# Kernel optimization log

Measured on AMD Instinct MI355X. Metric: run time of the kernel, lower is better.

The kernel has to match this reference:

```python
import jax, jax.numpy as jnp
import numpy as np

IN_NF, IN_EF, OUT_NF, H1, H2, H_IN = 16, 8, 16, 8, 8, 16
N_NODES, N_EDGES = 100000, 2000000


def _mlp(x, w1, b1, w2, b2):
    # Linear -> LeakyReLU(0.2) -> Linear
    return jax.nn.leaky_relu(x @ w1 + b1, negative_slope=0.2) @ w2 + b2


def setup_inputs() -> dict:
    key = jax.random.key(0)
    ks = jax.random.split(key, 20)
    d_in = 2 * IN_NF + IN_EF  # 40
    inp = {
        "nf": jax.random.normal(ks[0], (N_NODES, IN_NF), jnp.float32),
        "src_out": jax.random.randint(ks[1], (N_EDGES,), 0, N_NODES),
        "dst_out": jax.random.randint(ks[2], (N_EDGES,), 0, N_NODES),
        "nef_out": jax.random.normal(ks[3], (N_EDGES, IN_EF), jnp.float32),
        "src_in": jax.random.randint(ks[4], (N_EDGES,), 0, N_NODES),
        "dst_in": jax.random.randint(ks[5], (N_EDGES,), 0, N_NODES),
        "nef_in": jax.random.normal(ks[6], (N_EDGES, IN_EF), jnp.float32),
        # MLP_msg_o2i: (2*in_nf+in_ef) -> h_in -> out_nf
        "w_o2i1": jax.random.normal(ks[7], (d_in, H_IN), jnp.float32) * 0.1,
        "b_o2i1": jnp.zeros((H_IN,), jnp.float32),
        "w_o2i2": jax.random.normal(ks[8], (H_IN, OUT_NF), jnp.float32) * 0.1,
        "b_o2i2": jnp.zeros((OUT_NF,), jnp.float32),
        # MLP_msg_i2o: (2*in_nf+in_ef) -> h_in -> 1+h1+h2
        "w_i2o1": jax.random.normal(ks[9], (d_in, H_IN), jnp.float32) * 0.1,
        "b_i2o1": jnp.zeros((H_IN,), jnp.float32),
        "w_i2o2": jax.random.normal(ks[10], (H_IN, 1 + H1 + H2), jnp.float32) * 0.1,
        "b_i2o2": jnp.zeros((1 + H1 + H2,), jnp.float32),
        # MLP_reduce_o: (in_nf+h1+h2) -> h_in -> out_nf  (note: in_nf==out_nf here)
        "w_red1": jax.random.normal(ks[11], (OUT_NF + H1 + H2, H_IN), jnp.float32) * 0.1,
        "b_red1": jnp.zeros((H_IN,), jnp.float32),
        "w_red2": jax.random.normal(ks[12], (H_IN, OUT_NF), jnp.float32) * 0.1,
        "b_red2": jnp.zeros((OUT_NF,), jnp.float32),
    }
    return inp


def reference(nf, src_out, dst_out, nef_out, src_in, dst_in, nef_in,
              w_o2i1, b_o2i1, w_o2i2, b_o2i2,
              w_i2o1, b_i2o1, w_i2o2, b_i2o2,
              w_red1, b_red1, w_red2, b_red2):
    n = nf.shape[0]
    # --- update_all over 'net_out': edge gather-concat -> MLP -> scatter sum
    x_o = jnp.concatenate([nf[src_out], nf[dst_out], nef_out], axis=1)  # [E, 40]
    efi = _mlp(x_o, w_o2i1, b_o2i1, w_o2i2, b_o2i2)                      # [E, out_nf]
    new_nf = jax.ops.segment_sum(efi, dst_out, num_segments=n)           # overwrites 'new_nf'
    # --- apply_edges over 'net_in': gated messages
    x_i = jnp.concatenate([nf[src_in], nf[dst_in], nef_in], axis=1)      # [E, 40]
    m = _mlp(x_i, w_i2o1, b_i2o1, w_i2o2, b_i2o2)                        # [E, 1+h1+h2]
    k = jax.nn.sigmoid(m[:, :1])
    efo1 = m[:, 1:1 + H1] * k
    efo2 = m[:, 1 + H1:] * k
    # --- scatter sum / mean into dst nodes
    nfo1 = jax.ops.segment_sum(efo1, dst_in, num_segments=n)
    cnt = jax.ops.segment_sum(jnp.ones((dst_in.shape[0],), nf.dtype), dst_in, num_segments=n)
    nfo2 = jax.ops.segment_sum(efo2, dst_in, num_segments=n) / jnp.maximum(cnt, 1.0)[:, None]
    # --- apply_nodes only on net_in destination nodes; others keep new_nf
    reduced = _mlp(jnp.concatenate([new_nf, nfo1, nfo2], axis=1), w_red1, b_red1, w_red2, b_red2)
    has_in = (cnt > 0)[:, None]
    return jnp.where(has_in, reduced, new_nf)
```

## Files before the change

kernel.cpp:

```cpp
#include <hip/hip_runtime.h>
#include <math.h>

#define IN_NF 16
#define IN_EF 8
#define OUT_NF 16
#define H1 8
#define H2 8
#define H_IN 16
#define D_IN 40
#define NT 4
#define SCAN_NB 128

typedef unsigned int uivec4 __attribute__((ext_vector_type(4)));

__device__ __forceinline__ unsigned int f2bf_bits(float f) {
    unsigned int u = __float_as_uint(f);
    u += 0x7FFFu + ((u >> 16) & 1u);
    return u >> 16;
}
__device__ __forceinline__ float bf_lo(unsigned int w) { return __uint_as_float(w << 16); }
__device__ __forceinline__ float bf_hi(unsigned int w) { return __uint_as_float(w & 0xFFFF0000u); }

__global__ __launch_bounds__(256) void k_pre(
    const float* __restrict__ nf, unsigned short* __restrict__ nf16, int n_nodes,
    const int* __restrict__ dst_out, const int* __restrict__ dst_in,
    int* __restrict__ curA, int* __restrict__ curB, int n_edges, int nb_conv)
{
    if ((int)blockIdx.x < nb_conv) {
        int n = blockIdx.x * 256 + threadIdx.x;
        if (n >= n_nodes) return;
        const float4* p = (const float4*)(nf + (long)n * IN_NF);
        unsigned int w[8];
#pragma unroll
        for (int q = 0; q < 4; ++q) {
            float4 v = p[q];
            w[2*q+0] = f2bf_bits(v.x) | (f2bf_bits(v.y) << 16);
            w[2*q+1] = f2bf_bits(v.z) | (f2bf_bits(v.w) << 16);
        }
        uint4* o = (uint4*)(nf16 + (size_t)n * 16);
        o[0] = make_uint4(w[0], w[1], w[2], w[3]);
        o[1] = make_uint4(w[4], w[5], w[6], w[7]);
    } else {
        int i = ((blockIdx.x - nb_conv) * 256 + threadIdx.x) * 4;
        if (i + 3 < n_edges) {
            int4 a = *(const int4*)(dst_out + i);
            atomicAdd(&curA[a.x], 1); atomicAdd(&curA[a.y], 1);
            atomicAdd(&curA[a.z], 1); atomicAdd(&curA[a.w], 1);
            int4 b = *(const int4*)(dst_in + i);
            atomicAdd(&curB[b.x], 1); atomicAdd(&curB[b.y], 1);
            atomicAdd(&curB[b.z], 1); atomicAdd(&curB[b.w], 1);
        } else {
            for (int e = i; e < n_edges; ++e) {
                atomicAdd(&curA[dst_out[e]], 1);
                atomicAdd(&curB[dst_in[e]], 1);
            }
        }
    }
}

__global__ __launch_bounds__(256) void k_hist(
    const int* __restrict__ dst_out, const int* __restrict__ dst_in,
    int* __restrict__ off_out, int* __restrict__ off_in, int n_edges)
{
    int i = (blockIdx.x * blockDim.x + threadIdx.x) * 4;
    if (i + 3 < n_edges) {
        int4 a = *(const int4*)(dst_out + i);
        atomicAdd(&off_out[a.x], 1); atomicAdd(&off_out[a.y], 1);
        atomicAdd(&off_out[a.z], 1); atomicAdd(&off_out[a.w], 1);
        int4 b = *(const int4*)(dst_in + i);
        atomicAdd(&off_in[b.x], 1); atomicAdd(&off_in[b.y], 1);
        atomicAdd(&off_in[b.z], 1); atomicAdd(&off_in[b.w], 1);
    } else {
        for (int e = i; e < n_edges; ++e) {
            atomicAdd(&off_out[dst_out[e]], 1);
            atomicAdd(&off_in[dst_in[e]], 1);
        }
    }
}

__global__ __launch_bounds__(256) void k_scan_partial(
    const int* __restrict__ a0, const int* __restrict__ a1, int n,
    int* __restrict__ bsum)
{
    int arr = blockIdx.x >> 7;
    int blk = blockIdx.x & (SCAN_NB - 1);
    const int* a = arr ? a1 : a0;
    int chunk = (n + SCAN_NB - 1) / SCAN_NB;
    int beg = blk * chunk;
    int end = min(beg + chunk, n);
    int s = 0;
    for (int i = beg + threadIdx.x; i < end; i += 256) s += a[i];
    __shared__ int sm[256];
    int t = threadIdx.x;
    sm[t] = s;
    __syncthreads();
    for (int d = 128; d > 0; d >>= 1) {
        if (t < d) sm[t] += sm[t + d];
        __syncthreads();
    }
    if (t == 0) bsum[arr * SCAN_NB + blk] = sm[0];
}

__global__ __launch_bounds__(64) void k_scan_bsum(int* __restrict__ bsum)
{
    int arr = threadIdx.x;
    if (arr >= 2) return;
    int run = 0;
    for (int i = 0; i < SCAN_NB; ++i) {
        int v = bsum[arr * SCAN_NB + i];
        bsum[arr * SCAN_NB + i] = run;
        run += v;
    }
}

__global__ __launch_bounds__(256) void k_scan_final(
    int* __restrict__ a0, int* __restrict__ a1, int n,
    const int* __restrict__ bsum)
{
    int arr = blockIdx.x >> 7;
    int blk = blockIdx.x & (SCAN_NB - 1);
    int* a = arr ? a1 : a0;
    int chunk = (n + SCAN_NB - 1) / SCAN_NB;
    int beg = blk * chunk;
    int end = min(beg + chunk, n);
    int t = threadIdx.x;
    __shared__ int sm[256];
    __shared__ int carry_sm;
    if (t == 0) carry_sm = bsum[arr * SCAN_NB + blk];
    __syncthreads();
    for (int base = beg; base < end; base += 256) {
        int i = base + t;
        int v = (i < end) ? a[i] : 0;
        sm[t] = v;
        __syncthreads();
        for (int d = 1; d < 256; d <<= 1) {
            int u = (t >= d) ? sm[t - d] : 0;
            __syncthreads();
            sm[t] += u;
            __syncthreads();
        }
        int carry = carry_sm;
        if (i < end) a[i] = carry + sm[t] - v;
        __syncthreads();
        if (t == 0) carry_sm = carry + sm[255];
        __syncthreads();
    }
}

__global__ __launch_bounds__(256, 4) void k_edges(
    const unsigned short* __restrict__ nf16,
    const int* __restrict__ srcA, const int* __restrict__ dstA,
    const float* __restrict__ nefA,
    const int* __restrict__ srcB, const int* __restrict__ dstB,
    const float* __restrict__ nefB,
    const float* __restrict__ W1A, const float* __restrict__ B1A,
    const float* __restrict__ W2A, const float* __restrict__ B2A,
    const float* __restrict__ W1B, const float* __restrict__ B1B,
    const float* __restrict__ W2B, const float* __restrict__ B2B,
    int* __restrict__ curA, int* __restrict__ curB,
    unsigned short* __restrict__ msgA, unsigned short* __restrict__ msgB,
    int n_edges, int nbe)
{
    bool isA = (int)blockIdx.x < nbe;
    int bid = isA ? (int)blockIdx.x : (int)blockIdx.x - nbe;
    int e = bid * 256 + (int)threadIdx.x;
    if (e >= n_edges) return;

    const int* src = isA ? srcA : srcB;
    const int* dst = isA ? dstA : dstB;
    const float* nef = isA ? nefA : nefB;
    const float* W1 = isA ? W1A : W1B;
    const float* B1 = isA ? B1A : B1B;
    int* cursor = isA ? curA : curB;
    unsigned short* msg = isA ? msgA : msgB;

    int s = src[e];
    int d = dst[e];

    const uint4* pS = (const uint4*)(nf16 + (size_t)s * 16);
    uint4 Sa = pS[0], Sb = pS[1];
    const uint4* pD = (const uint4*)(nf16 + (size_t)d * 16);
    uint4 Da = pD[0], Db = pD[1];
    const float4* pN = (const float4*)(nef + (size_t)e * IN_EF);
    float4 Na = pN[0], Nb = pN[1];

    int slot = atomicAdd(&cursor[d], 1);

    float h[H_IN];
#pragma unroll
    for (int j = 0; j < H_IN; ++j) h[j] = B1[j];
    {
        unsigned int wS[8] = {Sa.x,Sa.y,Sa.z,Sa.w,Sb.x,Sb.y,Sb.z,Sb.w};
        unsigned int wD[8] = {Da.x,Da.y,Da.z,Da.w,Db.x,Db.y,Db.z,Db.w};
#pragma unroll
        for (int w = 0; w < 8; ++w) {
            float a0 = bf_lo(wS[w]), a1 = bf_hi(wS[w]);
            float b0 = bf_lo(wD[w]), b1 = bf_hi(wD[w]);
            const float* r0 = W1 + (2*w) * H_IN;
            const float* r1 = W1 + (2*w+1) * H_IN;
            const float* r2 = W1 + (IN_NF + 2*w) * H_IN;
            const float* r3 = W1 + (IN_NF + 2*w+1) * H_IN;
#pragma unroll
            for (int j = 0; j < H_IN; ++j) {
                h[j] = fmaf(a0, r0[j], h[j]);
                h[j] = fmaf(a1, r1[j], h[j]);
                h[j] = fmaf(b0, r2[j], h[j]);
                h[j] = fmaf(b1, r3[j], h[j]);
            }
        }
        float nv[8] = {Na.x,Na.y,Na.z,Na.w,Nb.x,Nb.y,Nb.z,Nb.w};
#pragma unroll
        for (int k = 0; k < IN_EF; ++k) {
            const float* r = W1 + (2*IN_NF + k) * H_IN;
            float a0 = nv[k];
#pragma unroll
            for (int j = 0; j < H_IN; ++j) h[j] = fmaf(a0, r[j], h[j]);
        }
    }
#pragma unroll
    for (int j = 0; j < H_IN; ++j) h[j] = (h[j] >= 0.f) ? h[j] : 0.2f * h[j];

    unsigned int w[8];
    if (isA) {
        float o[OUT_NF];
#pragma unroll
        for (int j = 0; j < OUT_NF; ++j) o[j] = B2A[j];
#pragma unroll
        for (int k = 0; k < H_IN; ++k) {
            float hk = h[k];
            const float* r = W2A + k * OUT_NF;
#pragma unroll
            for (int j = 0; j < OUT_NF; ++j) o[j] = fmaf(hk, r[j], o[j]);
        }
#pragma unroll
        for (int q = 0; q < 8; ++q)
            w[q] = f2bf_bits(o[2*q]) | (f2bf_bits(o[2*q+1]) << 16);
    } else {
        const int M = 1 + H1 + H2;
        float o[17];
#pragma unroll
        for (int j = 0; j < M; ++j) o[j] = B2B[j];
#pragma unroll
        for (int k = 0; k < H_IN; ++k) {
            float hk = h[k];
            const float* r = W2B + k * M;
#pragma unroll
            for (int j = 0; j < M; ++j) o[j] = fmaf(hk, r[j], o[j]);
        }
        float g = 1.f / (1.f + __expf(-o[0]));
#pragma unroll
        for (int q = 0; q < 8; ++q)
            w[q] = f2bf_bits(o[1+2*q] * g) | (f2bf_bits(o[2+2*q] * g) << 16);
    }

    uivec4* pm = (uivec4*)(msg + (size_t)slot * 16);
    uivec4 v0 = {w[0], w[1], w[2], w[3]};
    uivec4 v1 = {w[4], w[5], w[6], w[7]};
    __builtin_nontemporal_store(v0, pm);
    __builtin_nontemporal_store(v1, pm + 1);
}

__global__ __launch_bounds__(256, 4) void k_gather(
    const int* __restrict__ curA, const int* __restrict__ curB,
    const unsigned short* __restrict__ msgA, const unsigned short* __restrict__ msgB,
    const float* __restrict__ w_red1, const float* __restrict__ b_red1,
    const float* __restrict__ w_red2, const float* __restrict__ b_red2,
    float* __restrict__ out, int n_nodes)
{
    int tid = blockIdx.x * blockDim.x + threadIdx.x;
    int node = tid >> 2;
    int t = tid & (NT - 1);
    if (node >= n_nodes) return;

    int begA = (node == 0) ? 0 : curA[node - 1];
    int endA = curA[node];
    int begB = (node == 0) ? 0 : curB[node - 1];
    int endB = curB[node];

    float accA[16], accB[16];
#pragma unroll
    for (int j = 0; j < 16; ++j) { accA[j] = 0.f; accB[j] = 0.f; }

    for (int i = begA + t; i < endA; i += NT) {
        const uint4* p = (const uint4*)(msgA + (size_t)i * 16);
        uint4 v0 = p[0], v1 = p[1];
        unsigned int w0=v0.x,w1=v0.y,w2=v0.z,w3=v0.w,w4=v1.x,w5=v1.y,w6=v1.z,w7=v1.w;
        accA[0]+=bf_lo(w0); accA[1]+=bf_hi(w0); accA[2]+=bf_lo(w1); accA[3]+=bf_hi(w1);
        accA[4]+=bf_lo(w2); accA[5]+=bf_hi(w2); accA[6]+=bf_lo(w3); accA[7]+=bf_hi(w3);
        accA[8]+=bf_lo(w4); accA[9]+=bf_hi(w4); accA[10]+=bf_lo(w5); accA[11]+=bf_hi(w5);
        accA[12]+=bf_lo(w6); accA[13]+=bf_hi(w6); accA[14]+=bf_lo(w7); accA[15]+=bf_hi(w7);
    }
    for (int i = begB + t; i < endB; i += NT) {
        const uint4* p = (const uint4*)(msgB + (size_t)i * 16);
        uint4 v0 = p[0], v1 = p[1];
        unsigned int w0=v0.x,w1=v0.y,w2=v0.z,w3=v0.w,w4=v1.x,w5=v1.y,w6=v1.z,w7=v1.w;
        accB[0]+=bf_lo(w0); accB[1]+=bf_hi(w0); accB[2]+=bf_lo(w1); accB[3]+=bf_hi(w1);
        accB[4]+=bf_lo(w2); accB[5]+=bf_hi(w2); accB[6]+=bf_lo(w3); accB[7]+=bf_hi(w3);
        accB[8]+=bf_lo(w4); accB[9]+=bf_hi(w4); accB[10]+=bf_lo(w5); accB[11]+=bf_hi(w5);
        accB[12]+=bf_lo(w6); accB[13]+=bf_hi(w6); accB[14]+=bf_lo(w7); accB[15]+=bf_hi(w7);
    }

#pragma unroll
    for (int mask = 1; mask < NT; mask <<= 1) {
#pragma unroll
        for (int j = 0; j < 16; ++j) {
            accA[j] += __shfl_xor(accA[j], mask);
            accB[j] += __shfl_xor(accB[j], mask);
        }
    }
    if (t != 0) return;

    int deg = endB - begB;
    float inv = 1.f / fmaxf((float)deg, 1.f);
    float x2[32];
#pragma unroll
    for (int j = 0; j < 16; ++j) x2[j] = accA[j];
#pragma unroll
    for (int j = 0; j < H1; ++j) x2[16 + j] = accB[j];
#pragma unroll
    for (int j = 0; j < H2; ++j) x2[16 + H1 + j] = accB[8 + j] * inv;

    float h[H_IN];
#pragma unroll
    for (int j = 0; j < H_IN; ++j) h[j] = b_red1[j];
#pragma unroll
    for (int k = 0; k < 32; ++k) {
        float xk = x2[k];
#pragma unroll
        for (int j = 0; j < H_IN; ++j) h[j] = fmaf(xk, w_red1[k * H_IN + j], h[j]);
    }
#pragma unroll
    for (int j = 0; j < H_IN; ++j) h[j] = (h[j] >= 0.f) ? h[j] : 0.2f * h[j];

    float o[OUT_NF];
#pragma unroll
    for (int j = 0; j < OUT_NF; ++j) o[j] = b_red2[j];
#pragma unroll
    for (int k = 0; k < H_IN; ++k) {
        float hk = h[k];
#pragma unroll
        for (int j = 0; j < OUT_NF; ++j) o[j] = fmaf(hk, w_red2[k * OUT_NF + j], o[j]);
    }

    bool has_in = (deg > 0);
    float4* po = (float4*)(out + (long)node * OUT_NF);
#pragma unroll
    for (int i = 0; i < 4; ++i) {
        float4 v;
        if (has_in) { v.x=o[4*i+0]; v.y=o[4*i+1]; v.z=o[4*i+2]; v.w=o[4*i+3]; }
        else        { v.x=accA[4*i+0]; v.y=accA[4*i+1]; v.z=accA[4*i+2]; v.w=accA[4*i+3]; }
        po[i] = v;
    }
}

__global__ __launch_bounds__(256) void k_scatter(
    const int* __restrict__ dst_out, const int* __restrict__ dst_in,
    int* __restrict__ off_out, int* __restrict__ off_in,
    int* __restrict__ perm_out, int* __restrict__ perm_in, int n_edges)
{
    int e = blockIdx.x * blockDim.x + threadIdx.x;
    if (e >= n_edges) return;
    int p0 = atomicAdd(&off_out[dst_out[e]], 1);
    perm_out[p0] = e;
    int p1 = atomicAdd(&off_in[dst_in[e]], 1);
    perm_in[p1] = e;
}

__global__ __launch_bounds__(256) void k_node_fused(
    const float* __restrict__ nf,
    const int* __restrict__ src_out, const float* __restrict__ nef_out,
    const int* __restrict__ src_in, const float* __restrict__ nef_in,
    const int* __restrict__ off_out, const int* __restrict__ off_in,
    const int* __restrict__ perm_out, const int* __restrict__ perm_in,
    const float* __restrict__ w_o2i1, const float* __restrict__ b_o2i1,
    const float* __restrict__ w_o2i2, const float* __restrict__ b_o2i2,
    const float* __restrict__ w_i2o1, const float* __restrict__ b_i2o1,
    const float* __restrict__ w_i2o2, const float* __restrict__ b_i2o2,
    const float* __restrict__ w_red1, const float* __restrict__ b_red1,
    const float* __restrict__ w_red2, const float* __restrict__ b_red2,
    float* __restrict__ out, int n_nodes)
{
    int tid = blockIdx.x * blockDim.x + threadIdx.x;
    int node = tid >> 2;
    int t = tid & (NT - 1);
    if (node >= n_nodes) return;

    float xd[IN_NF];
    {
        const float4* p = (const float4*)(nf + (long)node * IN_NF);
#pragma unroll
        for (int i = 0; i < 4; ++i) {
            float4 v = p[i];
            xd[4*i+0]=v.x; xd[4*i+1]=v.y; xd[4*i+2]=v.z; xd[4*i+3]=v.w;
        }
    }
    float hbA[H_IN], hbB[H_IN];
#pragma unroll
    for (int j = 0; j < H_IN; ++j) { hbA[j] = b_o2i1[j]; hbB[j] = b_i2o1[j]; }
#pragma unroll
    for (int k = 0; k < IN_NF; ++k) {
        float xk = xd[k];
#pragma unroll
        for (int j = 0; j < H_IN; ++j) {
            hbA[j] = fmaf(xk, w_o2i1[(IN_NF + k) * H_IN + j], hbA[j]);
            hbB[j] = fmaf(xk, w_i2o1[(IN_NF + k) * H_IN + j], hbB[j]);
        }
    }

    float accA[OUT_NF];
#pragma unroll
    for (int j = 0; j < OUT_NF; ++j) accA[j] = 0.f;
    int begO = (node == 0) ? 0 : off_out[node - 1];
    int endO = off_out[node];
    int localO = 0;
    for (int i = begO + t; i < endO; i += NT) {
        int e = perm_out[i];
        int s = src_out[e];
        float xs[IN_NF], xe[IN_EF];
        {
            const float4* ps = (const float4*)(nf + (long)s * IN_NF);
#pragma unroll
            for (int q = 0; q < 4; ++q) {
                float4 v = ps[q];
                xs[4*q+0]=v.x; xs[4*q+1]=v.y; xs[4*q+2]=v.z; xs[4*q+3]=v.w;
            }
            const float4* pe = (const float4*)(nef_out + (long)e * IN_EF);
#pragma unroll
            for (int q = 0; q < 2; ++q) {
                float4 v = pe[q];
                xe[4*q+0]=v.x; xe[4*q+1]=v.y; xe[4*q+2]=v.z; xe[4*q+3]=v.w;
            }
        }
        float h[H_IN];
#pragma unroll
        for (int j = 0; j < H_IN; ++j) h[j] = hbA[j];
#pragma unroll
        for (int k = 0; k < IN_NF; ++k) {
            float xk = xs[k];
#pragma unroll
            for (int j = 0; j < H_IN; ++j) h[j] = fmaf(xk, w_o2i1[k * H_IN + j], h[j]);
        }
#pragma unroll
        for (int k = 0; k < IN_EF; ++k) {
            float xk = xe[k];
#pragma unroll
            for (int j = 0; j < H_IN; ++j) h[j] = fmaf(xk, w_o2i1[(2*IN_NF + k) * H_IN + j], h[j]);
        }
#pragma unroll
        for (int j = 0; j < H_IN; ++j) h[j] = (h[j] >= 0.f) ? h[j] : 0.2f * h[j];
#pragma unroll
        for (int k = 0; k < H_IN; ++k) {
            float hk = h[k];
#pragma unroll
            for (int j = 0; j < OUT_NF; ++j) accA[j] = fmaf(hk, w_o2i2[k * OUT_NF + j], accA[j]);
        }
        ++localO;
    }
#pragma unroll
    for (int j = 0; j < OUT_NF; ++j) accA[j] = fmaf((float)localO, b_o2i2[j], accA[j]);

    float acc1[H1], acc2[H2];
#pragma unroll
    for (int j = 0; j < H1; ++j) acc1[j] = 0.f;
#pragma unroll
    for (int j = 0; j < H2; ++j) acc2[j] = 0.f;
    int begI = (node == 0) ? 0 : off_in[node - 1];
    int endI = off_in[node];
    int deg = endI - begI;
    for (int i = begI + t; i < endI; i += NT) {
        int e = perm_in[i];
        int s = src_in[e];
        float xs[IN_NF], xe[IN_EF];
        {
            const float4* ps = (const float4*)(nf + (long)s * IN_NF);
#pragma unroll
            for (int q = 0; q < 4; ++q) {
                float4 v = ps[q];
                xs[4*q+0]=v.x; xs[4*q+1]=v.y; xs[4*q+2]=v.z; xs[4*q+3]=v.w;
            }
            const float4* pe = (const float4*)(nef_in + (long)e * IN_EF);
#pragma unroll
            for (int q = 0; q < 2; ++q) {
                float4 v = pe[q];
                xe[4*q+0]=v.x; xe[4*q+1]=v.y; xe[4*q+2]=v.z; xe[4*q+3]=v.w;
            }
        }
        float h[H_IN];
#pragma unroll
        for (int j = 0; j < H_IN; ++j) h[j] = hbB[j];
#pragma unroll
        for (int k = 0; k < IN_NF; ++k) {
            float xk = xs[k];
#pragma unroll
            for (int j = 0; j < H_IN; ++j) h[j] = fmaf(xk, w_i2o1[k * H_IN + j], h[j]);
        }
#pragma unroll
        for (int k = 0; k < IN_EF; ++k) {
            float xk = xe[k];
#pragma unroll
            for (int j = 0; j < H_IN; ++j) h[j] = fmaf(xk, w_i2o1[(2*IN_NF + k) * H_IN + j], h[j]);
        }
#pragma unroll
        for (int j = 0; j < H_IN; ++j) h[j] = (h[j] >= 0.f) ? h[j] : 0.2f * h[j];

        const int M = 1 + H1 + H2;
        float o[17];
#pragma unroll
        for (int j = 0; j < M; ++j) o[j] = b_i2o2[j];
#pragma unroll
        for (int k = 0; k < H_IN; ++k) {
            float hk = h[k];
#pragma unroll
            for (int j = 0; j < M; ++j) o[j] = fmaf(hk, w_i2o2[k * M + j], o[j]);
        }
        float gate = 1.f / (1.f + __expf(-o[0]));
#pragma unroll
        for (int j = 0; j < H1; ++j) acc1[j] = fmaf(o[1 + j], gate, acc1[j]);
#pragma unroll
        for (int j = 0; j < H2; ++j) acc2[j] = fmaf(o[1 + H1 + j], gate, acc2[j]);
    }

#pragma unroll
    for (int mask = 1; mask < NT; mask <<= 1) {
#pragma unroll
        for (int j = 0; j < OUT_NF; ++j) accA[j] += __shfl_xor(accA[j], mask);
#pragma unroll
        for (int j = 0; j < H1; ++j) acc1[j] += __shfl_xor(acc1[j], mask);
#pragma unroll
        for (int j = 0; j < H2; ++j) acc2[j] += __shfl_xor(acc2[j], mask);
    }
    if (t != 0) return;

    float inv = 1.f / fmaxf((float)deg, 1.f);
    float x2[32];
#pragma unroll
    for (int j = 0; j < OUT_NF; ++j) x2[j] = accA[j];
#pragma unroll
    for (int j = 0; j < H1; ++j) x2[OUT_NF + j] = acc1[j];
#pragma unroll
    for (int j = 0; j < H2; ++j) x2[OUT_NF + H1 + j] = acc2[j] * inv;

    float h[H_IN];
#pragma unroll
    for (int j = 0; j < H_IN; ++j) h[j] = b_red1[j];
#pragma unroll
    for (int k = 0; k < 32; ++k) {
        float xk = x2[k];
#pragma unroll
        for (int j = 0; j < H_IN; ++j) h[j] = fmaf(xk, w_red1[k * H_IN + j], h[j]);
    }
#pragma unroll
    for (int j = 0; j < H_IN; ++j) h[j] = (h[j] >= 0.f) ? h[j] : 0.2f * h[j];

    float o[OUT_NF];
#pragma unroll
    for (int j = 0; j < OUT_NF; ++j) o[j] = b_red2[j];
#pragma unroll
    for (int k = 0; k < H_IN; ++k) {
        float hk = h[k];
#pragma unroll
        for (int j = 0; j < OUT_NF; ++j) o[j] = fmaf(hk, w_red2[k * OUT_NF + j], o[j]);
    }

    bool has_in = (deg > 0);
    float4* po = (float4*)(out + (long)node * OUT_NF);
#pragma unroll
    for (int i = 0; i < 4; ++i) {
        float4 v;
        if (has_in) { v.x=o[4*i+0]; v.y=o[4*i+1]; v.z=o[4*i+2]; v.w=o[4*i+3]; }
        else        { v.x=accA[4*i+0]; v.y=accA[4*i+1]; v.z=accA[4*i+2]; v.w=accA[4*i+3]; }
        po[i] = v;
    }
}

extern "C" void kernel_launch(void* const* d_in, const int* in_sizes, int n_in,
                              void* d_out, int out_size, void* d_ws, size_t ws_size,
                              hipStream_t stream) {
    const float* nf      = (const float*)d_in[0];
    const int*   src_out = (const int*)d_in[1];
    const int*   dst_out = (const int*)d_in[2];
    const float* nef_out = (const float*)d_in[3];
    const int*   src_in  = (const int*)d_in[4];
    const int*   dst_in  = (const int*)d_in[5];
    const float* nef_in  = (const float*)d_in[6];
    const float* w_o2i1  = (const float*)d_in[7];
    const float* b_o2i1  = (const float*)d_in[8];
    const float* w_o2i2  = (const float*)d_in[9];
    const float* b_o2i2  = (const float*)d_in[10];
    const float* w_i2o1  = (const float*)d_in[11];
    const float* b_i2o1  = (const float*)d_in[12];
    const float* w_i2o2  = (const float*)d_in[13];
    const float* b_i2o2  = (const float*)d_in[14];
    const float* w_red1  = (const float*)d_in[15];
    const float* b_red1  = (const float*)d_in[16];
    const float* w_red2  = (const float*)d_in[17];
    const float* b_red2  = (const float*)d_in[18];

    int n_nodes = in_sizes[0] / IN_NF;
    int n_edges = in_sizes[1];
    float* out = (float*)d_out;

    dim3 blk(256);
    dim3 egrid((n_edges + 255) / 256);
    dim3 hgrid((n_edges / 4 + 256) / 256 + 1);
    dim3 ngrid(((size_t)n_nodes * NT + 255) / 256);
    dim3 sgrid(2 * SCAN_NB);

    size_t off_bytes = (size_t)2 * n_nodes * sizeof(int);
    size_t nf16_bytes = (size_t)n_nodes * 16 * sizeof(unsigned short);
    size_t msg_bytes = (size_t)n_edges * 16 * sizeof(unsigned short);
    size_t need_fast = off_bytes + nf16_bytes + 2 * msg_bytes + 256;

    if (ws_size >= need_fast) {
        int* curA = (int*)d_ws;
        int* curB = curA + n_nodes;
        unsigned short* nf16 = (unsigned short*)(curB + n_nodes);
        unsigned short* msgA = nf16 + (size_t)n_nodes * 16;
        unsigned short* msgB = msgA + (size_t)n_edges * 16;
        int* bsum = (int*)msgA;

        int nb_conv = (n_nodes + 255) / 256;
        int nb_hist = (n_edges / 4 + 256) / 256 + 1;
        dim3 pgrid(nb_conv + nb_hist);

        int nbe = (n_edges + 255) / 256;
        dim3 edge_grid(2 * nbe);

        hipMemsetAsync(d_ws, 0, off_bytes, stream);
        k_pre<<<pgrid, blk, 0, stream>>>(nf, nf16, n_nodes, dst_out, dst_in,
                                         curA, curB, n_edges, nb_conv);
        k_scan_partial<<<sgrid, blk, 0, stream>>>(curA, curB, n_nodes, bsum);
        k_scan_bsum<<<dim3(1), dim3(64), 0, stream>>>(bsum);
        k_scan_final<<<sgrid, blk, 0, stream>>>(curA, curB, n_nodes, bsum);
        k_edges<<<edge_grid, blk, 0, stream>>>(nf16,
                                               src_out, dst_out, nef_out,
                                               src_in, dst_in, nef_in,
                                               w_o2i1, b_o2i1, w_o2i2, b_o2i2,
                                               w_i2o1, b_i2o1, w_i2o2, b_i2o2,
                                               curA, curB, msgA, msgB,
                                               n_edges, nbe);
        k_gather<<<ngrid, blk, 0, stream>>>(curA, curB, msgA, msgB,
                                            w_red1, b_red1, w_red2, b_red2,
                                            out, n_nodes);
    } else {
        int* off_out  = (int*)d_ws;
        int* off_in   = off_out + n_nodes;
        int* perm_out = off_in + n_nodes;
        int* perm_in  = perm_out + n_edges;
        int* bsum = perm_out;

        hipMemsetAsync(d_ws, 0, off_bytes, stream);
        k_hist<<<hgrid, blk, 0, stream>>>(dst_out, dst_in, off_out, off_in, n_edges);
        k_scan_partial<<<sgrid, blk, 0, stream>>>(off_out, off_in, n_nodes, bsum);
        k_scan_bsum<<<dim3(1), dim3(64), 0, stream>>>(bsum);
        k_scan_final<<<sgrid, blk, 0, stream>>>(off_out, off_in, n_nodes, bsum);
        k_scatter<<<egrid, blk, 0, stream>>>(dst_out, dst_in, off_out, off_in,
                                             perm_out, perm_in, n_edges);
        k_node_fused<<<ngrid, blk, 0, stream>>>(nf, src_out, nef_out, src_in, nef_in,
                                          off_out, off_in, perm_out, perm_in,
                                          w_o2i1, b_o2i1, w_o2i2, b_o2i2,
                                          w_i2o1, b_i2o1, w_i2o2, b_i2o2,
                                          w_red1, b_red1, w_red2, b_red2,
                                          out, n_nodes);
    }
}
```

Baseline: 458.5 us.

## Write edge messages in edge order and gather via inverse slot index

The edge kernel now writes each bf16 message at its own edge index in a plain streaming pattern, and it records the edge id at the node-sorted slot in a new inverse index array. The gather kernel then reads each node's messages through this index instead of reading a contiguous CSR-ordered buffer. The aim is to replace scattered 32-byte message stores with coalesced stores. In exchange the gather does indirect 32-byte reads, and each edge costs an extra 4-byte scattered write. The old CSR path is kept as the fallback when the workspace is too small, and the older perm-based fallback is removed.

```diff
diff --git a/kernel.cpp b/kernel.cpp
--- a/kernel.cpp
+++ b/kernel.cpp
@@ -7,7 +7,6 @@
 #define H1 8
 #define H2 8
 #define H_IN 16
-#define D_IN 40
 #define NT 4
 #define SCAN_NB 128
 
@@ -54,26 +53,6 @@
                 atomicAdd(&curA[dst_out[e]], 1);
                 atomicAdd(&curB[dst_in[e]], 1);
             }
-        }
-    }
-}
-
-__global__ __launch_bounds__(256) void k_hist(
-    const int* __restrict__ dst_out, const int* __restrict__ dst_in,
-    int* __restrict__ off_out, int* __restrict__ off_in, int n_edges)
-{
-    int i = (blockIdx.x * blockDim.x + threadIdx.x) * 4;
-    if (i + 3 < n_edges) {
-        int4 a = *(const int4*)(dst_out + i);
-        atomicAdd(&off_out[a.x], 1); atomicAdd(&off_out[a.y], 1);
-        atomicAdd(&off_out[a.z], 1); atomicAdd(&off_out[a.w], 1);
-        int4 b = *(const int4*)(dst_in + i);
-        atomicAdd(&off_in[b.x], 1); atomicAdd(&off_in[b.y], 1);
-        atomicAdd(&off_in[b.z], 1); atomicAdd(&off_in[b.w], 1);
-    } else {
-        for (int e = i; e < n_edges; ++e) {
-            atomicAdd(&off_out[dst_out[e]], 1);
-            atomicAdd(&off_in[dst_in[e]], 1);
         }
     }
 }
@@ -147,7 +126,231 @@
     }
 }
 
-__global__ __launch_bounds__(256, 4) void k_edges(
+__global__ __launch_bounds__(256, 4) void k_edges_stream(
+    const unsigned short* __restrict__ nf16,
+    const int* __restrict__ srcA, const int* __restrict__ dstA,
+    const float* __restrict__ nefA,
+    const int* __restrict__ srcB, const int* __restrict__ dstB,
+    const float* __restrict__ nefB,
+    const float* __restrict__ W1A, const float* __restrict__ B1A,
+    const float* __restrict__ W2A, const float* __restrict__ B2A,
+    const float* __restrict__ W1B, const float* __restrict__ B1B,
+    const float* __restrict__ W2B, const float* __restrict__ B2B,
+    int* __restrict__ curA, int* __restrict__ curB,
+    int* __restrict__ invA, int* __restrict__ invB,
+    unsigned short* __restrict__ msgA, unsigned short* __restrict__ msgB,
+    int n_edges, int nbe)
+{
+    bool isA = (int)blockIdx.x < nbe;
+    int bid = isA ? (int)blockIdx.x : (int)blockIdx.x - nbe;
+    int e = bid * 256 + (int)threadIdx.x;
+    if (e >= n_edges) return;
+
+    const int* src = isA ? srcA : srcB;
+    const int* dst = isA ? dstA : dstB;
+    const float* nef = isA ? nefA : nefB;
+    const float* W1 = isA ? W1A : W1B;
+    const float* B1 = isA ? B1A : B1B;
+    int* cursor = isA ? curA : curB;
+    int* inv = isA ? invA : invB;
+    unsigned short* msg = isA ? msgA : msgB;
+
+    int s = src[e];
+    int d = dst[e];
+
+    const uint4* pS = (const uint4*)(nf16 + (size_t)s * 16);
+    uint4 Sa = pS[0], Sb = pS[1];
+    const uint4* pD = (const uint4*)(nf16 + (size_t)d * 16);
+    uint4 Da = pD[0], Db = pD[1];
+    const float4* pN = (const float4*)(nef + (size_t)e * IN_EF);
+    float4 Na = pN[0], Nb = pN[1];
+
+    int slot = atomicAdd(&cursor[d], 1);
+
+    float h[H_IN];
+#pragma unroll
+    for (int j = 0; j < H_IN; ++j) h[j] = B1[j];
+    {
+        unsigned int wS[8] = {Sa.x,Sa.y,Sa.z,Sa.w,Sb.x,Sb.y,Sb.z,Sb.w};
+        unsigned int wD[8] = {Da.x,Da.y,Da.z,Da.w,Db.x,Db.y,Db.z,Db.w};
+#pragma unroll
+        for (int w = 0; w < 8; ++w) {
+            float a0 = bf_lo(wS[w]), a1 = bf_hi(wS[w]);
+            float b0 = bf_lo(wD[w]), b1 = bf_hi(wD[w]);
+            const float* r0 = W1 + (2*w) * H_IN;
+            const float* r1 = W1 + (2*w+1) * H_IN;
+            const float* r2 = W1 + (IN_NF + 2*w) * H_IN;
+            const float* r3 = W1 + (IN_NF + 2*w+1) * H_IN;
+#pragma unroll
+            for (int j = 0; j < H_IN; ++j) {
+                h[j] = fmaf(a0, r0[j], h[j]);
+                h[j] = fmaf(a1, r1[j], h[j]);
+                h[j] = fmaf(b0, r2[j], h[j]);
+                h[j] = fmaf(b1, r3[j], h[j]);
+            }
+        }
+        float nv[8] = {Na.x,Na.y,Na.z,Na.w,Nb.x,Nb.y,Nb.z,Nb.w};
+#pragma unroll
+        for (int k = 0; k < IN_EF; ++k) {
+            const float* r = W1 + (2*IN_NF + k) * H_IN;
+            float a0 = nv[k];
+#pragma unroll
+            for (int j = 0; j < H_IN; ++j) h[j] = fmaf(a0, r[j], h[j]);
+        }
+    }
+#pragma unroll
+    for (int j = 0; j < H_IN; ++j) h[j] = (h[j] >= 0.f) ? h[j] : 0.2f * h[j];
+
+    unsigned int w[8];
+    if (isA) {
+        float o[OUT_NF];
+#pragma unroll
+        for (int j = 0; j < OUT_NF; ++j) o[j] = B2A[j];
+#pragma unroll
+        for (int k = 0; k < H_IN; ++k) {
+            float hk = h[k];
+            const float* r = W2A + k * OUT_NF;
+#pragma unroll
+            for (int j = 0; j < OUT_NF; ++j) o[j] = fmaf(hk, r[j], o[j]);
+        }
+#pragma unroll
+        for (int q = 0; q < 8; ++q)
+            w[q] = f2bf_bits(o[2*q]) | (f2bf_bits(o[2*q+1]) << 16);
+    } else {
+        const int M = 1 + H1 + H2;
+        float o[17];
+#pragma unroll
+        for (int j = 0; j < M; ++j) o[j] = B2B[j];
+#pragma unroll
+        for (int k = 0; k < H_IN; ++k) {
+            float hk = h[k];
+            const float* r = W2B + k * M;
+#pragma unroll
+            for (int j = 0; j < M; ++j) o[j] = fmaf(hk, r[j], o[j]);
+        }
+        float g = 1.f / (1.f + __expf(-o[0]));
+#pragma unroll
+        for (int q = 0; q < 8; ++q)
+            w[q] = f2bf_bits(o[1+2*q] * g) | (f2bf_bits(o[2+2*q] * g) << 16);
+    }
+
+    uivec4* pm = (uivec4*)(msg + (size_t)e * 16);
+    uivec4 v0 = {w[0], w[1], w[2], w[3]};
+    uivec4 v1 = {w[4], w[5], w[6], w[7]};
+    __builtin_nontemporal_store(v0, pm);
+    __builtin_nontemporal_store(v1, pm + 1);
+    inv[slot] = e;
+}
+
+__global__ __launch_bounds__(256, 4) void k_gather_ind(
+    const int* __restrict__ curA, const int* __restrict__ curB,
+    const int* __restrict__ invA, const int* __restrict__ invB,
+    const unsigned short* __restrict__ msgA, const unsigned short* __restrict__ msgB,
+    const float* __restrict__ w_red1, const float* __restrict__ b_red1,
+    const float* __restrict__ w_red2, const float* __restrict__ b_red2,
+    float* __restrict__ out, int n_nodes)
+{
+    int tid = blockIdx.x * blockDim.x + threadIdx.x;
+    int node = tid >> 2;
+    int t = tid & (NT - 1);
+    if (node >= n_nodes) return;
+
+    int begA = (node == 0) ? 0 : curA[node - 1];
+    int endA = curA[node];
+    int begB = (node == 0) ? 0 : curB[node - 1];
+    int endB = curB[node];
+
+    float accA[16], accB[16];
+#pragma unroll
+    for (int j = 0; j < 16; ++j) { accA[j] = 0.f; accB[j] = 0.f; }
+
+    {
+        int i = begA + t;
+        int e = (i < endA) ? invA[i] : 0;
+        while (i < endA) {
+            int inext = i + NT;
+            int enext = (inext < endA) ? invA[inext] : 0;
+            const uint4* p = (const uint4*)(msgA + (size_t)e * 16);
+            uint4 v0 = p[0], v1 = p[1];
+            unsigned int w0=v0.x,w1=v0.y,w2=v0.z,w3=v0.w,w4=v1.x,w5=v1.y,w6=v1.z,w7=v1.w;
+            accA[0]+=bf_lo(w0); accA[1]+=bf_hi(w0); accA[2]+=bf_lo(w1); accA[3]+=bf_hi(w1);
+            accA[4]+=bf_lo(w2); accA[5]+=bf_hi(w2); accA[6]+=bf_lo(w3); accA[7]+=bf_hi(w3);
+            accA[8]+=bf_lo(w4); accA[9]+=bf_hi(w4); accA[10]+=bf_lo(w5); accA[11]+=bf_hi(w5);
+            accA[12]+=bf_lo(w6); accA[13]+=bf_hi(w6); accA[14]+=bf_lo(w7); accA[15]+=bf_hi(w7);
+            i = inext; e = enext;
+        }
+    }
+    {
+        int i = begB + t;
+        int e = (i < endB) ? invB[i] : 0;
+        while (i < endB) {
+            int inext = i + NT;
+            int enext = (inext < endB) ? invB[inext] : 0;
+            const uint4* p = (const uint4*)(msgB + (size_t)e * 16);
+            uint4 v0 = p[0], v1 = p[1];
+            unsigned int w0=v0.x,w1=v0.y,w2=v0.z,w3=v0.w,w4=v1.x,w5=v1.y,w6=v1.z,w7=v1.w;
+            accB[0]+=bf_lo(w0); accB[1]+=bf_hi(w0); accB[2]+=bf_lo(w1); accB[3]+=bf_hi(w1);
+            accB[4]+=bf_lo(w2); accB[5]+=bf_hi(w2); accB[6]+=bf_lo(w3); accB[7]+=bf_hi(w3);
+            accB[8]+=bf_lo(w4); accB[9]+=bf_hi(w4); accB[10]+=bf_lo(w5); accB[11]+=bf_hi(w5);
+            accB[12]+=bf_lo(w6); accB[13]+=bf_hi(w6); accB[14]+=bf_lo(w7); accB[15]+=bf_hi(w7);
+            i = inext; e = enext;
+        }
+    }
+
+#pragma unroll
+    for (int mask = 1; mask < NT; mask <<= 1) {
+#pragma unroll
+        for (int j = 0; j < 16; ++j) {
+            accA[j] += __shfl_xor(accA[j], mask);
+            accB[j] += __shfl_xor(accB[j], mask);
+        }
+    }
+    if (t != 0) return;
+
+    int deg = endB - begB;
+    float inv = 1.f / fmaxf((float)deg, 1.f);
+    float x2[32];
+#pragma unroll
+    for (int j = 0; j < 16; ++j) x2[j] = accA[j];
+#pragma unroll
+    for (int j = 0; j < H1; ++j) x2[16 + j] = accB[j];
+#pragma unroll
+    for (int j = 0; j < H2; ++j) x2[16 + H1 + j] = accB[8 + j] * inv;
+
+    float h[H_IN];
+#pragma unroll
+    for (int j = 0; j < H_IN; ++j) h[j] = b_red1[j];
+#pragma unroll
+    for (int k = 0; k < 32; ++k) {
+        float xk = x2[k];
+#pragma unroll
+        for (int j = 0; j < H_IN; ++j) h[j] = fmaf(xk, w_red1[k * H_IN + j], h[j]);
+    }
+#pragma unroll
+    for (int j = 0; j < H_IN; ++j) h[j] = (h[j] >= 0.f) ? h[j] : 0.2f * h[j];
+
+    float o[OUT_NF];
+#pragma unroll
+    for (int j = 0; j < OUT_NF; ++j) o[j] = b_red2[j];
+#pragma unroll
+    for (int k = 0; k < H_IN; ++k) {
+        float hk = h[k];
+#pragma unroll
+        for (int j = 0; j < OUT_NF; ++j) o[j] = fmaf(hk, w_red2[k * OUT_NF + j], o[j]);
+    }
+
+    bool has_in = (deg > 0);
+    float4* po = (float4*)(out + (long)node * OUT_NF);
+#pragma unroll
+    for (int i = 0; i < 4; ++i) {
+        float4 v;
+        if (has_in) { v.x=o[4*i+0]; v.y=o[4*i+1]; v.z=o[4*i+2]; v.w=o[4*i+3]; }
+        else        { v.x=accA[4*i+0]; v.y=accA[4*i+1]; v.z=accA[4*i+2]; v.w=accA[4*i+3]; }
+        po[i] = v;
+    }
+}
+
+__global__ __launch_bounds__(256, 4) void k_edges_csr(
     const unsigned short* __restrict__ nf16,
     const int* __restrict__ srcA, const int* __restrict__ dstA,
     const float* __restrict__ nefA,
@@ -260,7 +463,7 @@
     __builtin_nontemporal_store(v1, pm + 1);
 }
 
-__global__ __launch_bounds__(256, 4) void k_gather(
+__global__ __launch_bounds__(256, 4) void k_gather_csr(
     const int* __restrict__ curA, const int* __restrict__ curB,
     const unsigned short* __restrict__ msgA, const unsigned short* __restrict__ msgB,
     const float* __restrict__ w_red1, const float* __restrict__ b_red1,
@@ -319,226 +522,6 @@
     for (int j = 0; j < H1; ++j) x2[16 + j] = accB[j];
 #pragma unroll
     for (int j = 0; j < H2; ++j) x2[16 + H1 + j] = accB[8 + j] * inv;
-
-    float h[H_IN];
-#pragma unroll
-    for (int j = 0; j < H_IN; ++j) h[j] = b_red1[j];
-#pragma unroll
-    for (int k = 0; k < 32; ++k) {
-        float xk = x2[k];
-#pragma unroll
-        for (int j = 0; j < H_IN; ++j) h[j] = fmaf(xk, w_red1[k * H_IN + j], h[j]);
-    }
-#pragma unroll
-    for (int j = 0; j < H_IN; ++j) h[j] = (h[j] >= 0.f) ? h[j] : 0.2f * h[j];
-
-    float o[OUT_NF];
-#pragma unroll
-    for (int j = 0; j < OUT_NF; ++j) o[j] = b_red2[j];
-#pragma unroll
-    for (int k = 0; k < H_IN; ++k) {
-        float hk = h[k];
-#pragma unroll
-        for (int j = 0; j < OUT_NF; ++j) o[j] = fmaf(hk, w_red2[k * OUT_NF + j], o[j]);
-    }
-
-    bool has_in = (deg > 0);
-    float4* po = (float4*)(out + (long)node * OUT_NF);
-#pragma unroll
-    for (int i = 0; i < 4; ++i) {
-        float4 v;
-        if (has_in) { v.x=o[4*i+0]; v.y=o[4*i+1]; v.z=o[4*i+2]; v.w=o[4*i+3]; }
-        else        { v.x=accA[4*i+0]; v.y=accA[4*i+1]; v.z=accA[4*i+2]; v.w=accA[4*i+3]; }
-        po[i] = v;
-    }
-}
-
-__global__ __launch_bounds__(256) void k_scatter(
-    const int* __restrict__ dst_out, const int* __restrict__ dst_in,
-    int* __restrict__ off_out, int* __restrict__ off_in,
-    int* __restrict__ perm_out, int* __restrict__ perm_in, int n_edges)
-{
-    int e = blockIdx.x * blockDim.x + threadIdx.x;
-    if (e >= n_edges) return;
-    int p0 = atomicAdd(&off_out[dst_out[e]], 1);
-    perm_out[p0] = e;
-    int p1 = atomicAdd(&off_in[dst_in[e]], 1);
-    perm_in[p1] = e;
-}
-
-__global__ __launch_bounds__(256) void k_node_fused(
-    const float* __restrict__ nf,
-    const int* __restrict__ src_out, const float* __restrict__ nef_out,
-    const int* __restrict__ src_in, const float* __restrict__ nef_in,
-    const int* __restrict__ off_out, const int* __restrict__ off_in,
-    const int* __restrict__ perm_out, const int* __restrict__ perm_in,
-    const float* __restrict__ w_o2i1, const float* __restrict__ b_o2i1,
-    const float* __restrict__ w_o2i2, const float* __restrict__ b_o2i2,
-    const float* __restrict__ w_i2o1, const float* __restrict__ b_i2o1,
-    const float* __restrict__ w_i2o2, const float* __restrict__ b_i2o2,
-    const float* __restrict__ w_red1, const float* __restrict__ b_red1,
-    const float* __restrict__ w_red2, const float* __restrict__ b_red2,
-    float* __restrict__ out, int n_nodes)
-{
-    int tid = blockIdx.x * blockDim.x + threadIdx.x;
-    int node = tid >> 2;
-    int t = tid & (NT - 1);
-    if (node >= n_nodes) return;
-
-    float xd[IN_NF];
-    {
-        const float4* p = (const float4*)(nf + (long)node * IN_NF);
-#pragma unroll
-        for (int i = 0; i < 4; ++i) {
-            float4 v = p[i];
-            xd[4*i+0]=v.x; xd[4*i+1]=v.y; xd[4*i+2]=v.z; xd[4*i+3]=v.w;
-        }
-    }
-    float hbA[H_IN], hbB[H_IN];
-#pragma unroll
-    for (int j = 0; j < H_IN; ++j) { hbA[j] = b_o2i1[j]; hbB[j] = b_i2o1[j]; }
-#pragma unroll
-    for (int k = 0; k < IN_NF; ++k) {
-        float xk = xd[k];
-#pragma unroll
-        for (int j = 0; j < H_IN; ++j) {
-            hbA[j] = fmaf(xk, w_o2i1[(IN_NF + k) * H_IN + j], hbA[j]);
-            hbB[j] = fmaf(xk, w_i2o1[(IN_NF + k) * H_IN + j], hbB[j]);
-        }
-    }
-
-    float accA[OUT_NF];
-#pragma unroll
-    for (int j = 0; j < OUT_NF; ++j) accA[j] = 0.f;
-    int begO = (node == 0) ? 0 : off_out[node - 1];
-    int endO = off_out[node];
-    int localO = 0;
-    for (int i = begO + t; i < endO; i += NT) {
-        int e = perm_out[i];
-        int s = src_out[e];
-        float xs[IN_NF], xe[IN_EF];
-        {
-            const float4* ps = (const float4*)(nf + (long)s * IN_NF);
-#pragma unroll
-            for (int q = 0; q < 4; ++q) {
-                float4 v = ps[q];
-                xs[4*q+0]=v.x; xs[4*q+1]=v.y; xs[4*q+2]=v.z; xs[4*q+3]=v.w;
-            }
-            const float4* pe = (const float4*)(nef_out + (long)e * IN_EF);
-#pragma unroll
-            for (int q = 0; q < 2; ++q) {
-                float4 v = pe[q];
-                xe[4*q+0]=v.x; xe[4*q+1]=v.y; xe[4*q+2]=v.z; xe[4*q+3]=v.w;
-            }
-        }
-        float h[H_IN];
-#pragma unroll
-        for (int j = 0; j < H_IN; ++j) h[j] = hbA[j];
-#pragma unroll
-        for (int k = 0; k < IN_NF; ++k) {
-            float xk = xs[k];
-#pragma unroll
-            for (int j = 0; j < H_IN; ++j) h[j] = fmaf(xk, w_o2i1[k * H_IN + j], h[j]);
-        }
-#pragma unroll
-        for (int k = 0; k < IN_EF; ++k) {
-            float xk = xe[k];
-#pragma unroll
-            for (int j = 0; j < H_IN; ++j) h[j] = fmaf(xk, w_o2i1[(2*IN_NF + k) * H_IN + j], h[j]);
-        }
-#pragma unroll
-        for (int j = 0; j < H_IN; ++j) h[j] = (h[j] >= 0.f) ? h[j] : 0.2f * h[j];
-#pragma unroll
-        for (int k = 0; k < H_IN; ++k) {
-            float hk = h[k];
-#pragma unroll
-            for (int j = 0; j < OUT_NF; ++j) accA[j] = fmaf(hk, w_o2i2[k * OUT_NF + j], accA[j]);
-        }
-        ++localO;
-    }
-#pragma unroll
-    for (int j = 0; j < OUT_NF; ++j) accA[j] = fmaf((float)localO, b_o2i2[j], accA[j]);
-
-    float acc1[H1], acc2[H2];
-#pragma unroll
-    for (int j = 0; j < H1; ++j) acc1[j] = 0.f;
-#pragma unroll
-    for (int j = 0; j < H2; ++j) acc2[j] = 0.f;
-    int begI = (node == 0) ? 0 : off_in[node - 1];
-    int endI = off_in[node];
-    int deg = endI - begI;
-    for (int i = begI + t; i < endI; i += NT) {
-        int e = perm_in[i];
-        int s = src_in[e];
-        float xs[IN_NF], xe[IN_EF];
-        {
-            const float4* ps = (const float4*)(nf + (long)s * IN_NF);
-#pragma unroll
-            for (int q = 0; q < 4; ++q) {
-                float4 v = ps[q];
-                xs[4*q+0]=v.x; xs[4*q+1]=v.y; xs[4*q+2]=v.z; xs[4*q+3]=v.w;
-            }
-            const float4* pe = (const float4*)(nef_in + (long)e * IN_EF);
-#pragma unroll
-            for (int q = 0; q < 2; ++q) {
-                float4 v = pe[q];
-                xe[4*q+0]=v.x; xe[4*q+1]=v.y; xe[4*q+2]=v.z; xe[4*q+3]=v.w;
-            }
-        }
-        float h[H_IN];
-#pragma unroll
-        for (int j = 0; j < H_IN; ++j) h[j] = hbB[j];
-#pragma unroll
-        for (int k = 0; k < IN_NF; ++k) {
-            float xk = xs[k];
-#pragma unroll
-            for (int j = 0; j < H_IN; ++j) h[j] = fmaf(xk, w_i2o1[k * H_IN + j], h[j]);
-        }
-#pragma unroll
-        for (int k = 0; k < IN_EF; ++k) {
-            float xk = xe[k];
-#pragma unroll
-            for (int j = 0; j < H_IN; ++j) h[j] = fmaf(xk, w_i2o1[(2*IN_NF + k) * H_IN + j], h[j]);
-        }
-#pragma unroll
-        for (int j = 0; j < H_IN; ++j) h[j] = (h[j] >= 0.f) ? h[j] : 0.2f * h[j];
-
-        const int M = 1 + H1 + H2;
-        float o[17];
-#pragma unroll
-        for (int j = 0; j < M; ++j) o[j] = b_i2o2[j];
-#pragma unroll
-        for (int k = 0; k < H_IN; ++k) {
-            float hk = h[k];
-#pragma unroll
-            for (int j = 0; j < M; ++j) o[j] = fmaf(hk, w_i2o2[k * M + j], o[j]);
-        }
-        float gate = 1.f / (1.f + __expf(-o[0]));
-#pragma unroll
-        for (int j = 0; j < H1; ++j) acc1[j] = fmaf(o[1 + j], gate, acc1[j]);
-#pragma unroll
-        for (int j = 0; j < H2; ++j) acc2[j] = fmaf(o[1 + H1 + j], gate, acc2[j]);
-    }
-
-#pragma unroll
-    for (int mask = 1; mask < NT; mask <<= 1) {
-#pragma unroll
-        for (int j = 0; j < OUT_NF; ++j) accA[j] += __shfl_xor(accA[j], mask);
-#pragma unroll
-        for (int j = 0; j < H1; ++j) acc1[j] += __shfl_xor(acc1[j], mask);
-#pragma unroll
-        for (int j = 0; j < H2; ++j) acc2[j] += __shfl_xor(acc2[j], mask);
-    }
-    if (t != 0) return;
-
-    float inv = 1.f / fmaxf((float)deg, 1.f);
-    float x2[32];
-#pragma unroll
-    for (int j = 0; j < OUT_NF; ++j) x2[j] = accA[j];
-#pragma unroll
-    for (int j = 0; j < H1; ++j) x2[OUT_NF + j] = acc1[j];
-#pragma unroll
-    for (int j = 0; j < H2; ++j) x2[OUT_NF + H1 + j] = acc2[j] * inv;
 
     float h[H_IN];
 #pragma unroll
@@ -601,17 +584,49 @@
     float* out = (float*)d_out;
 
     dim3 blk(256);
-    dim3 egrid((n_edges + 255) / 256);
-    dim3 hgrid((n_edges / 4 + 256) / 256 + 1);
     dim3 ngrid(((size_t)n_nodes * NT + 255) / 256);
     dim3 sgrid(2 * SCAN_NB);
 
-    size_t off_bytes = (size_t)2 * n_nodes * sizeof(int);
+    size_t off_bytes  = (size_t)2 * n_nodes * sizeof(int);
     size_t nf16_bytes = (size_t)n_nodes * 16 * sizeof(unsigned short);
-    size_t msg_bytes = (size_t)n_edges * 16 * sizeof(unsigned short);
-    size_t need_fast = off_bytes + nf16_bytes + 2 * msg_bytes + 256;
-
-    if (ws_size >= need_fast) {
+    size_t inv_bytes  = (size_t)n_edges * sizeof(int);
+    size_t msg_bytes  = (size_t)n_edges * 16 * sizeof(unsigned short);
+    size_t need2 = off_bytes + nf16_bytes + 2 * inv_bytes + 2 * msg_bytes + 256;
+
+    int nb_conv = (n_nodes + 255) / 256;
+    int nb_hist = (n_edges / 4 + 256) / 256 + 1;
+    dim3 pgrid(nb_conv + nb_hist);
+    int nbe = (n_edges + 255) / 256;
+    dim3 edge_grid(2 * nbe);
+
+    if (ws_size >= need2) {
+        int* curA = (int*)d_ws;
+        int* curB = curA + n_nodes;
+        unsigned short* nf16 = (unsigned short*)(curB + n_nodes);
+        int* invA = (int*)(nf16 + (size_t)n_nodes * 16);
+        int* invB = invA + n_edges;
+        unsigned short* msgA = (unsigned short*)(invB + n_edges);
+        unsigned short* msgB = msgA + (size_t)n_edges * 16;
+        int* bsum = (int*)msgA;
+
+        hipMemsetAsync(d_ws, 0, off_bytes, stream);
+        k_pre<<<pgrid, blk, 0, stream>>>(nf, nf16, n_nodes, dst_out, dst_in,
+                                         curA, curB, n_edges, nb_conv);
+        k_scan_partial<<<sgrid, blk, 0, stream>>>(curA, curB, n_nodes, bsum);
+        k_scan_bsum<<<dim3(1), dim3(64), 0, stream>>>(bsum);
+        k_scan_final<<<sgrid, blk, 0, stream>>>(curA, curB, n_nodes, bsum);
+        k_edges_stream<<<edge_grid, blk, 0, stream>>>(nf16,
+                                               src_out, dst_out, nef_out,
+                                               src_in, dst_in, nef_in,
+                                               w_o2i1, b_o2i1, w_o2i2, b_o2i2,
+                                               w_i2o1, b_i2o1, w_i2o2, b_i2o2,
+                                               curA, curB, invA, invB,
+                                               msgA, msgB, n_edges, nbe);
+        k_gather_ind<<<ngrid, blk, 0, stream>>>(curA, curB, invA, invB,
+                                            msgA, msgB,
+                                            w_red1, b_red1, w_red2, b_red2,
+                                            out, n_nodes);
+    } else {
         int* curA = (int*)d_ws;
         int* curB = curA + n_nodes;
         unsigned short* nf16 = (unsigned short*)(curB + n_nodes);
@@ -619,48 +634,21 @@
         unsigned short* msgB = msgA + (size_t)n_edges * 16;
         int* bsum = (int*)msgA;
 
-        int nb_conv = (n_nodes + 255) / 256;
-        int nb_hist = (n_edges / 4 + 256) / 256 + 1;
-        dim3 pgrid(nb_conv + nb_hist);
-
-        int nbe = (n_edges + 255) / 256;
-        dim3 edge_grid(2 * nbe);
-
         hipMemsetAsync(d_ws, 0, off_bytes, stream);
         k_pre<<<pgrid, blk, 0, stream>>>(nf, nf16, n_nodes, dst_out, dst_in,
                                          curA, curB, n_edges, nb_conv);
         k_scan_partial<<<sgrid, blk, 0, stream>>>(curA, curB, n_nodes, bsum);
         k_scan_bsum<<<dim3(1), dim3(64), 0, stream>>>(bsum);
         k_scan_final<<<sgrid, blk, 0, stream>>>(curA, curB, n_nodes, bsum);
-        k_edges<<<edge_grid, blk, 0, stream>>>(nf16,
+        k_edges_csr<<<edge_grid, blk, 0, stream>>>(nf16,
                                                src_out, dst_out, nef_out,
                                                src_in, dst_in, nef_in,
                                                w_o2i1, b_o2i1, w_o2i2, b_o2i2,
                                                w_i2o1, b_i2o1, w_i2o2, b_i2o2,
                                                curA, curB, msgA, msgB,
                                                n_edges, nbe);
-        k_gather<<<ngrid, blk, 0, stream>>>(curA, curB, msgA, msgB,
+        k_gather_csr<<<ngrid, blk, 0, stream>>>(curA, curB, msgA, msgB,
                                             w_red1, b_red1, w_red2, b_red2,
                                             out, n_nodes);
-    } else {
-        int* off_out  = (int*)d_ws;
-        int* off_in   = off_out + n_nodes;
-        int* perm_out = off_in + n_nodes;
-        int* perm_in  = perm_out + n_edges;
-        int* bsum = perm_out;
-
-        hipMemsetAsync(d_ws, 0, off_bytes, stream);
-        k_hist<<<hgrid, blk, 0, stream>>>(dst_out, dst_in, off_out, off_in, n_edges);
-        k_scan_partial<<<sgrid, blk, 0, stream>>>(off_out, off_in, n_nodes, bsum);
-        k_scan_bsum<<<dim3(1), dim3(64), 0, stream>>>(bsum);
-        k_scan_final<<<sgrid, blk, 0, stream>>>(off_out, off_in, n_nodes, bsum);
-        k_scatter<<<egrid, blk, 0, stream>>>(dst_out, dst_in, off_out, off_in,
-                                             perm_out, perm_in, n_edges);
-        k_node_fused<<<ngrid, blk, 0, stream>>>(nf, src_out, nef_out, src_in, nef_in,
-                                          off_out, off_in, perm_out, perm_in,
-                                          w_o2i1, b_o2i1, w_o2i2, b_o2i2,
-                                          w_i2o1, b_i2o1, w_i2o2, b_i2o2,
-                                          w_red1, b_red1, w_red2, b_red2,
-                                          out, n_nodes);
-    }
-}
+    }
+}
```

Result: slower. 566.8 us (+23.6%).
